# Kernel optimization log

Measured on AMD Instinct MI355X. Metric: run time of the kernel, lower is better.

Reference implementation:

```python
import jax, jax.numpy as jnp
import numpy as np

N, S, D = 8, 1024, 512      # batch, seq_len, in_dim
H, KD, VD, OD = 8, 64, 64, 512  # heads, key_dim, value_dim, out_dim
GRAPH_WEIGHT = 0.5
NEG_INF = float('-inf')


def setup_inputs() -> dict:
    key = jax.random.key(0)
    ks = jax.random.split(key, 9)
    return {
        "x":    jax.random.normal(ks[0], (N, S, D), jnp.float32),
        "Wk":   jax.random.normal(ks[1], (H, D, KD), jnp.float32) * 0.02,
        "bk":   jax.random.normal(ks[2], (H, KD), jnp.float32) * 0.02,
        "Wv":   jax.random.normal(ks[3], (H, D, VD), jnp.float32) * 0.02,
        "bv":   jax.random.normal(ks[4], (H, VD), jnp.float32) * 0.02,
        "Wout": jax.random.normal(ks[5], (H * VD, OD), jnp.float32) * 0.02,
        "bout": jax.random.normal(ks[6], (OD,), jnp.float32) * 0.02,
        "graph": jax.random.normal(ks[7], (S, S), jnp.float32),
        "knn": 64,
    }


def reference(x, Wk, bk, Wv, bv, Wout, bout, graph, knn):
    # Per-head key/value projections (heads vectorized on leading axis h).
    k = jnp.einsum('nsd,hdk->hnsk', x, Wk) + bk[:, None, None, :]   # (H,N,S,KD)
    v = jnp.einsum('nsd,hdv->hnsv', x, Wv) + bv[:, None, None, :]   # (H,N,S,VD)
    q = k  # self-attention: query = key

    # att_unnorm = (q . k) / sqrt(key_dim)  -> (H,N,S,S)
    att = jnp.einsum('hnqk,hntk->hnqt', q, k) / np.sqrt(KD).astype(np.float32)

    # Causal mask (equivalent to the Python loop att[:, i, i+1:] = -inf).
    causal = jnp.tril(jnp.ones((S, S), dtype=bool))
    att = jnp.where(causal, att, NEG_INF)

    # knn top-k pooling: keep top-knn entries along the last axis, rest -> -inf.
    topv = jax.lax.top_k(att, knn)[0]                  # (H,N,S,knn)
    kth = topv[..., -1:]                               # kth largest per row
    att = jnp.where(att >= kth, att, NEG_INF)

    p = jax.nn.softmax(att, axis=-1)

    # Graph-weighted attention blend (graph is row-softmaxed at init time).
    att_graph = jax.nn.softmax(graph, axis=-1)         # (S,S)
    p = GRAPH_WEIGHT * att_graph + (1.0 - GRAPH_WEIGHT) * p

    # y_h = att @ value, then concat heads and output projection.
    y = jnp.einsum('hnqt,hntv->hnqv', p, v)            # (H,N,S,VD)
    y = y.transpose(1, 2, 0, 3).reshape(N, S, H * VD)  # head-major concat
    return y @ Wout + bout
```

## Files before the change

kernel.cpp:

```cpp
#include <hip/hip_runtime.h>
#include <math.h>

#define NB 8
#define SL 1024
#define DI 512
#define HH 8
#define KDN 64
#define VDN 64
#define ODN 512
#define ATT_SCALE 0.125f

#define KLO_OFF 2097152u
#define V_OFF   4194304u
#define G_OFF   8388608u
#define Y_OFF   9437184u

#define ORD_NEG_INF 0x007FFFFFu

typedef __attribute__((ext_vector_type(8))) short bf16x8;
typedef __attribute__((ext_vector_type(4))) float f32x4;

__device__ __forceinline__ unsigned fordu(float f) {
  unsigned b = __float_as_uint(f);
  return b ^ ((b & 0x80000000u) ? 0xFFFFFFFFu : 0x80000000u);
}
__device__ __forceinline__ float ifordu(unsigned k) {
  unsigned b = k ^ ((k & 0x80000000u) ? 0x80000000u : 0xFFFFFFFFu);
  return __uint_as_float(b);
}
__device__ __forceinline__ unsigned short f2bf(float f) {
  unsigned u = __float_as_uint(f);
  unsigned r = (u + 0x7FFFu + ((u >> 16) & 1u)) >> 16;
  return (unsigned short)r;
}
__device__ __forceinline__ float bf2f(unsigned short h) {
  return __uint_as_float(((unsigned)h) << 16);
}

__global__ __launch_bounds__(256) void wprep_kernel(
    const float* __restrict__ Wk, const float* __restrict__ Wv, float* __restrict__ ws)
{
  __shared__ float tile[64][65];
  unsigned short* gbase = (unsigned short*)(ws + G_OFF);
  const int t = threadIdx.x;
  const int d0 = blockIdx.x * 64;
  const int hs = blockIdx.y;
  const int h = hs & 7, which = hs >> 3;
  const float* W = (which == 0) ? (Wk + (size_t)h * DI * KDN) : (Wv + (size_t)h * DI * VDN);
  unsigned short* whi = gbase + (size_t)which * 524288 + (size_t)h * KDN * DI;
  unsigned short* wlo = whi + 262144;
  const int r = t >> 2, c4 = (t & 3) * 16;
#pragma unroll
  for (int j = 0; j < 4; ++j)
    *(float4*)&tile[r][c4 + j * 4] = *(const float4*)&W[(size_t)(d0 + r) * KDN + c4 + j * 4];
  __syncthreads();
  union { unsigned short u[16]; uint4 v[2]; } hi, lo;
#pragma unroll
  for (int j = 0; j < 16; ++j) {
    const float f = tile[c4 + j][r];
    const unsigned short h16 = f2bf(f);
    hi.u[j] = h16;
    lo.u[j] = f2bf(f - bf2f(h16));
  }
  const size_t o = (size_t)r * DI + d0 + c4;
  *(uint4*)&whi[o] = hi.v[0];
  *(uint4*)&whi[o + 8] = hi.v[1];
  *(uint4*)&wlo[o] = lo.v[0];
  *(uint4*)&wlo[o + 8] = lo.v[1];
}

__global__ __launch_bounds__(256) void kvproj_kernel(
    const float* __restrict__ x, const float* __restrict__ bk,
    const float* __restrict__ bv, float* __restrict__ ws)
{
  const unsigned short* gbase = (const unsigned short*)(ws + G_OFF);
  const unsigned short* wkthi = gbase;
  const unsigned short* wktlo = gbase + 262144;
  const unsigned short* wvthi = gbase + 524288;
  const unsigned short* wvtlo = gbase + 786432;
  unsigned short* khi = (unsigned short*)ws;
  unsigned short* klo = (unsigned short*)(ws + KLO_OFF);
  float* vb = ws + V_OFF;

  const int tid = threadIdx.x;
  const int lane = tid & 63;
  const int wave = tid >> 6;
  const int col = lane & 15, grp = lane >> 4;
  const int m0 = blockIdx.x * 64;
  const int h = blockIdx.y;
  const int n = m0 >> 10, s0 = m0 & 1023;

  f32x4 ack[4], acv[4];
#pragma unroll
  for (int odt = 0; odt < 4; ++odt) { ack[odt] = (f32x4){0,0,0,0}; acv[odt] = (f32x4){0,0,0,0}; }

  const float* xrow = x + (size_t)(m0 + wave * 16 + col) * DI + grp * 8;
  for (int ks = 0; ks < 16; ++ks) {
    const float4 ya = *(const float4*)&xrow[ks * 32];
    const float4 yb = *(const float4*)&xrow[ks * 32 + 4];
    union { unsigned short u[8]; bf16x8 v; } ah, al;
    const float yf[8] = {ya.x, ya.y, ya.z, ya.w, yb.x, yb.y, yb.z, yb.w};
#pragma unroll
    for (int j = 0; j < 8; ++j) {
      const unsigned short h16 = f2bf(yf[j]);
      ah.u[j] = h16;
      al.u[j] = f2bf(yf[j] - bf2f(h16));
    }
#pragma unroll
    for (int odt = 0; odt < 4; ++odt) {
      const size_t bo = (size_t)(h * 64 + odt * 16 + col) * DI + ks * 32 + grp * 8;
      const bf16x8 kh = *(const bf16x8*)&wkthi[bo];
      const bf16x8 kl = *(const bf16x8*)&wktlo[bo];
      ack[odt] = __builtin_amdgcn_mfma_f32_16x16x32_bf16(ah.v, kh, ack[odt], 0, 0, 0);
      ack[odt] = __builtin_amdgcn_mfma_f32_16x16x32_bf16(ah.v, kl, ack[odt], 0, 0, 0);
      ack[odt] = __builtin_amdgcn_mfma_f32_16x16x32_bf16(al.v, kh, ack[odt], 0, 0, 0);
      const bf16x8 vh = *(const bf16x8*)&wvthi[bo];
      const bf16x8 vl = *(const bf16x8*)&wvtlo[bo];
      acv[odt] = __builtin_amdgcn_mfma_f32_16x16x32_bf16(ah.v, vh, acv[odt], 0, 0, 0);
      acv[odt] = __builtin_amdgcn_mfma_f32_16x16x32_bf16(ah.v, vl, acv[odt], 0, 0, 0);
      acv[odt] = __builtin_amdgcn_mfma_f32_16x16x32_bf16(al.v, vh, acv[odt], 0, 0, 0);
    }
  }

  const size_t hnbase = ((size_t)(h * NB + n) * SL);
#pragma unroll
  for (int odt = 0; odt < 4; ++odt) {
    const int kd = odt * 16 + col;
    const float bkv = bk[h * KDN + kd];
    const float bvv = bv[h * VDN + kd];
#pragma unroll
    for (int r = 0; r < 4; ++r) {
      const int s = s0 + wave * 16 + grp * 4 + r;
      const float kf = ack[odt][r] + bkv;
      const unsigned short h16 = f2bf(kf);
      khi[(hnbase + s) * KDN + kd] = h16;
      klo[(hnbase + s) * KDN + kd] = f2bf(kf - bf2f(h16));
      vb[(hnbase + s) * VDN + kd] = acv[odt][r] + bvv;
    }
  }
}

__global__ __launch_bounds__(256) void gsoftmax_kernel(const float* __restrict__ gin, float* __restrict__ ws)
{
  unsigned short* ghi = (unsigned short*)(ws + G_OFF);
  const int row = blockIdx.x;
  const int tid = threadIdx.x;
  const int lane = tid & 63, wave = tid >> 6;
  __shared__ float red[4];
  __shared__ float red2[4];
  float v[4];
  float m = -INFINITY;
#pragma unroll
  for (int i = 0; i < 4; ++i) {
    v[i] = gin[(size_t)row * SL + tid + i * 256];
    m = fmaxf(m, v[i]);
  }
#pragma unroll
  for (int off = 32; off; off >>= 1) m = fmaxf(m, __shfl_xor(m, off));
  if (lane == 0) red[wave] = m;
  __syncthreads();
  m = fmaxf(fmaxf(red[0], red[1]), fmaxf(red[2], red[3]));
  float e[4];
  float s = 0.f;
#pragma unroll
  for (int i = 0; i < 4; ++i) { e[i] = __expf(v[i] - m); s += e[i]; }
#pragma unroll
  for (int off = 32; off; off >>= 1) s += __shfl_xor(s, off);
  if (lane == 0) red2[wave] = s;
  __syncthreads();
  s = red2[0] + red2[1] + red2[2] + red2[3];
  const float inv = 1.0f / s;
#pragma unroll
  for (int i = 0; i < 4; ++i) ghi[(size_t)row * SL + tid + i * 256] = f2bf(e[i] * inv);
}

__global__ __launch_bounds__(512, 8) void attn_kernel(float* __restrict__ ws, const int* __restrict__ knn_p)
{
  __shared__ float S[16][260];
  const int tid = threadIdx.x;
  const int lane = tid & 63;
  const int wave = tid >> 6;
  const int q0 = blockIdx.x * 16;
  const int hn = blockIdx.y;
  const int h = hn >> 3, n = hn & 7;
  const int K = knn_p[0];
  const unsigned short* khi = (const unsigned short*)ws + (size_t)hn * SL * KDN;
  const unsigned short* klo = (const unsigned short*)(ws + KLO_OFF) + (size_t)hn * SL * KDN;
  const float* vb = ws + V_OFF + (size_t)hn * (SL * VDN);
  float* y = ws + Y_OFF;

  const int col = lane & 15, grp = lane >> 4;
  const bf16x8 a0h = *(const bf16x8*)&khi[(size_t)(q0 + col) * KDN + grp * 8];
  const bf16x8 a1h = *(const bf16x8*)&khi[(size_t)(q0 + col) * KDN + 32 + grp * 8];
  const bf16x8 a0l = *(const bf16x8*)&klo[(size_t)(q0 + col) * KDN + grp * 8];
  const bf16x8 a1l = *(const bf16x8*)&klo[(size_t)(q0 + col) * KDN + 32 + grp * 8];

  const int T = q0 / 16 + 1;
  const int rbase = wave * 2;

  float ev[2][8][2];
#pragma unroll
  for (int rr = 0; rr < 2; ++rr)
#pragma unroll
    for (int c = 0; c < 8; ++c) {
      ev[rr][c][0] = __uint_as_float(ORD_NEG_INF);
      ev[rr][c][1] = __uint_as_float(ORD_NEG_INF);
    }

#pragma unroll
  for (int ph = 0; ph < 4; ++ph) {
    const int tlo = ph * 16;
    const int thi = (T < tlo + 16) ? T : (tlo + 16);
    if (thi > tlo) {
      __syncthreads();
      for (int ti = tlo + wave; ti < thi; ti += 8) {
        const int t0 = ti * 16;
        const size_t bo = (size_t)(t0 + col) * KDN + grp * 8;
        const bf16x8 b0h = *(const bf16x8*)&khi[bo];
        const bf16x8 b1h = *(const bf16x8*)&khi[bo + 32];
        const bf16x8 b0l = *(const bf16x8*)&klo[bo];
        const bf16x8 b1l = *(const bf16x8*)&klo[bo + 32];
        f32x4 d = {0.f, 0.f, 0.f, 0.f};
        d = __builtin_amdgcn_mfma_f32_16x16x32_bf16(a0h, b0h, d, 0, 0, 0);
        d = __builtin_amdgcn_mfma_f32_16x16x32_bf16(a1h, b1h, d, 0, 0, 0);
        d = __builtin_amdgcn_mfma_f32_16x16x32_bf16(a0h, b0l, d, 0, 0, 0);
        d = __builtin_amdgcn_mfma_f32_16x16x32_bf16(a1h, b1l, d, 0, 0, 0);
        d = __builtin_amdgcn_mfma_f32_16x16x32_bf16(a0l, b0h, d, 0, 0, 0);
        d = __builtin_amdgcn_mfma_f32_16x16x32_bf16(a1l, b1h, d, 0, 0, 0);
        d = __builtin_amdgcn_mfma_f32_16x16x32_bf16(a0l, b0l, d, 0, 0, 0);
        d = __builtin_amdgcn_mfma_f32_16x16x32_bf16(a1l, b1l, d, 0, 0, 0);
        const int tl = t0 - ph * 256 + col;
#pragma unroll
        for (int r = 0; r < 4; ++r) S[grp * 4 + r][tl] = d[r];
      }
      __syncthreads();
#pragma unroll
      for (int rr = 0; rr < 2; ++rr) {
        const int q = q0 + rbase + rr;
        const int cmr = q >> 7;
#pragma unroll
        for (int cc = 0; cc < 2; ++cc) {
          const int c = ph * 2 + cc;
          if (c <= cmr) {
            const float2 sv = *(const float2*)&S[rbase + rr][cc * 128 + lane * 2];
            const int t0 = c * 128 + lane * 2;
            const unsigned k0 = (t0     <= q) ? fordu(sv.x * ATT_SCALE) : ORD_NEG_INF;
            const unsigned k1 = (t0 + 1 <= q) ? fordu(sv.y * ATT_SCALE) : ORD_NEG_INF;
            ev[rr][c][0] = __uint_as_float(k0);
            ev[rr][c][1] = __uint_as_float(k1);
          }
        }
      }
    }
  }
  __syncthreads();

  float* elist = (float*)((char*)&S[0][0] + wave * 768);
  unsigned short* tlist = (unsigned short*)(elist + 128);

#pragma unroll
  for (int rr = 0; rr < 2; ++rr) {
    const int q = q0 + rbase + rr;

    unsigned u[16];
#pragma unroll
    for (int c = 0; c < 8; ++c) {
      u[c * 2]     = __float_as_uint(ev[rr][c][0]);
      u[c * 2 + 1] = __float_as_uint(ev[rr][c][1]);
    }

    unsigned lmax = u[0];
#pragma unroll
    for (int i = 1; i < 16; ++i) lmax = lmax > u[i] ? lmax : u[i];
    unsigned mk = lmax, t0k = lmax;
#pragma unroll
    for (int off = 32; off; off >>= 1) {
      const unsigned om = (unsigned)__shfl_xor((int)mk, off);
      const unsigned ot = (unsigned)__shfl_xor((int)t0k, off);
      mk = mk > om ? mk : om;
      t0k = t0k < ot ? t0k : ot;
    }
    const float m = ifordu(mk);

    unsigned kth;
    if (q < K) {
      kth = ORD_NEG_INF;
    } else {
      unsigned lo = (K <= 64) ? t0k : 0u;
      unsigned hi = mk;
      while (lo < hi) {
        const unsigned mid = lo + ((hi - lo + 1) >> 1);
        int cnt = 0;
#pragma unroll
        for (int i = 0; i < 16; ++i)
          cnt += (int)__popcll(__ballot(u[i] >= mid));
        if (cnt >= K) lo = mid; else hi = mid - 1;
      }
      kth = lo;
    }

    float Z = 0.f;
#pragma unroll
    for (int c = 0; c < 8; ++c) {
#pragma unroll
      for (int j = 0; j < 2; ++j) {
        const unsigned k = u[c * 2 + j];
        float e = 0.f;
        if (k >= kth) e = __expf(ifordu(k) - m);
        ev[rr][c][j] = e;
        Z += e;
      }
    }
#pragma unroll
    for (int off = 32; off; off >>= 1) Z += __shfl_xor(Z, off);

    const unsigned long long lt = (1ull << lane) - 1ull;
    int cnt = 0;
#pragma unroll
    for (int c = 0; c < 8; ++c) {
#pragma unroll
      for (int j = 0; j < 2; ++j) {
        const float e = ev[rr][c][j];
        const unsigned long long msk = __ballot(e > 0.f);
        if (e > 0.f) {
          const int pos = cnt + (int)__popcll(msk & lt);
          if (pos < 128) {
            elist[pos] = e;
            tlist[pos] = (unsigned short)(c * 128 + lane * 2 + j);
          }
        }
        cnt += (int)__popcll(msk);
      }
    }
    cnt = (cnt < 128) ? cnt : 128;

    float yacc = 0.f;
    int i2 = 0;
    for (; i2 + 4 <= cnt; i2 += 4) {
      const float4 e4 = *(const float4*)&elist[i2];
      const ushort4 t4 = *(const ushort4*)&tlist[i2];
      yacc = __fmaf_rn(e4.x, vb[(size_t)t4.x * VDN + lane], yacc);
      yacc = __fmaf_rn(e4.y, vb[(size_t)t4.y * VDN + lane], yacc);
      yacc = __fmaf_rn(e4.z, vb[(size_t)t4.z * VDN + lane], yacc);
      yacc = __fmaf_rn(e4.w, vb[(size_t)t4.w * VDN + lane], yacc);
    }
    for (; i2 < cnt; ++i2) {
      yacc = __fmaf_rn(elist[i2], vb[(size_t)tlist[i2] * VDN + lane], yacc);
    }
    y[((size_t)(n * SL + q)) * ODN + h * VDN + lane] = yacc * (0.5f / Z);
  }
}

__global__ __launch_bounds__(256) void vtprep_kernel(float* __restrict__ ws)
{
  __shared__ float tile[64][65];
  const int t = threadIdx.x;
  const int t0 = blockIdx.x * 64;
  const int hn = blockIdx.y;
  const float* vb = ws + V_OFF + (size_t)hn * (SL * VDN);
  unsigned short* vthi = (unsigned short*)ws + (size_t)hn * VDN * SL;
  const int r = t >> 2, c4 = (t & 3) * 16;
#pragma unroll
  for (int j = 0; j < 4; ++j)
    *(float4*)&tile[r][c4 + j * 4] = *(const float4*)&vb[(size_t)(t0 + r) * VDN + c4 + j * 4];
  __syncthreads();
  union { unsigned short u[16]; uint4 v[2]; } hi;
#pragma unroll
  for (int j = 0; j < 16; ++j) hi.u[j] = f2bf(tile[c4 + j][r]);
  const size_t o = (size_t)r * SL + t0 + c4;
  *(uint4*)&vthi[o] = hi.v[0];
  *(uint4*)&vthi[o + 8] = hi.v[1];
}

__global__ __launch_bounds__(256) void gv_kernel(float* __restrict__ ws)
{
  const unsigned short* ghi = (const unsigned short*)(ws + G_OFF);
  const int tid = threadIdx.x;
  const int lane = tid & 63;
  const int wave = tid >> 6;
  const int col = lane & 15, grp = lane >> 4;
  const int q0 = blockIdx.x * 64;
  const int hn = blockIdx.y;
  const int h = hn >> 3, n = hn & 7;
  const unsigned short* vthi = (const unsigned short*)ws + (size_t)hn * VDN * SL;
  float* y = ws + Y_OFF;

  f32x4 acc[4];
#pragma unroll
  for (int odt = 0; odt < 4; ++odt) acc[odt] = (f32x4){0.f, 0.f, 0.f, 0.f};

  const size_t arow = (size_t)(q0 + wave * 16 + col) * SL;
  for (int ks = 0; ks < 32; ++ks) {
    const bf16x8 ah = *(const bf16x8*)&ghi[arow + ks * 32 + grp * 8];
#pragma unroll
    for (int odt = 0; odt < 4; ++odt) {
      const bf16x8 bh = *(const bf16x8*)&vthi[(size_t)(odt * 16 + col) * SL + ks * 32 + grp * 8];
      acc[odt] = __builtin_amdgcn_mfma_f32_16x16x32_bf16(ah, bh, acc[odt], 0, 0, 0);
    }
  }

#pragma unroll
  for (int odt = 0; odt < 4; ++odt) {
    const int vd = odt * 16 + col;
#pragma unroll
    for (int r = 0; r < 4; ++r) {
      const size_t off = ((size_t)(n * SL + q0 + wave * 16 + grp * 4 + r)) * ODN + h * VDN + vd;
      y[off] += 0.5f * acc[odt][r];
    }
  }
}

__global__ __launch_bounds__(256) void wtprep_kernel(const float* __restrict__ Wout, float* __restrict__ ws)
{
  __shared__ float tile[64][65];
  unsigned short* wth = (unsigned short*)(ws + KLO_OFF);
  unsigned short* wtl = wth + ODN * ODN;
  const int t = threadIdx.x;
  const int od0 = blockIdx.x * 64;
  const int k0 = blockIdx.y * 64;
  const int r = t >> 2, c4 = (t & 3) * 16;
#pragma unroll
  for (int j = 0; j < 4; ++j) {
    *(float4*)&tile[r][c4 + j * 4] = *(const float4*)&Wout[(size_t)(k0 + r) * ODN + od0 + c4 + j * 4];
  }
  __syncthreads();
  union { unsigned short u[16]; uint4 v[2]; } hi, lo;
#pragma unroll
  for (int j = 0; j < 16; ++j) {
    const float f = tile[c4 + j][r];
    const unsigned short h16 = f2bf(f);
    hi.u[j] = h16;
    lo.u[j] = f2bf(f - bf2f(h16));
  }
  const size_t o = (size_t)(od0 + r) * ODN + k0 + c4;
  *(uint4*)&wth[o] = hi.v[0];
  *(uint4*)&wth[o + 8] = hi.v[1];
  *(uint4*)&wtl[o] = lo.v[0];
  *(uint4*)&wtl[o + 8] = lo.v[1];
}

__global__ __launch_bounds__(256) void out_kernel(
    const float* __restrict__ bout, const float* __restrict__ ws, float* __restrict__ out)
{
  const unsigned short* wth = (const unsigned short*)(ws + KLO_OFF);
  const unsigned short* wtl = wth + ODN * ODN;
  const float* y = ws + Y_OFF;
  const int tid = threadIdx.x;
  const int lane = tid & 63;
  const int wave = tid >> 6;
  const int col = lane & 15, grp = lane >> 4;
  const int od0 = blockIdx.x * 64;
  const int m0 = blockIdx.y * 64 + wave * 16;

  f32x4 acc[4];
#pragma unroll
  for (int odt = 0; odt < 4; ++odt) acc[odt] = (f32x4){0.f, 0.f, 0.f, 0.f};

  const float* yrow = y + (size_t)(m0 + col) * ODN + grp * 8;
  for (int ks = 0; ks < 16; ++ks) {
    const float4 ya = *(const float4*)&yrow[ks * 32];
    const float4 yb = *(const float4*)&yrow[ks * 32 + 4];
    union { unsigned short u[8]; bf16x8 v; } ah, al;
    const float yf[8] = {ya.x, ya.y, ya.z, ya.w, yb.x, yb.y, yb.z, yb.w};
#pragma unroll
    for (int j = 0; j < 8; ++j) {
      const unsigned short h16 = f2bf(yf[j]);
      ah.u[j] = h16;
      al.u[j] = f2bf(yf[j] - bf2f(h16));
    }
#pragma unroll
    for (int odt = 0; odt < 4; ++odt) {
      const size_t bo = (size_t)(od0 + odt * 16 + col) * ODN + ks * 32 + grp * 8;
      const bf16x8 bh = *(const bf16x8*)&wth[bo];
      const bf16x8 bl = *(const bf16x8*)&wtl[bo];
      acc[odt] = __builtin_amdgcn_mfma_f32_16x16x32_bf16(ah.v, bh, acc[odt], 0, 0, 0);
      acc[odt] = __builtin_amdgcn_mfma_f32_16x16x32_bf16(ah.v, bl, acc[odt], 0, 0, 0);
      acc[odt] = __builtin_amdgcn_mfma_f32_16x16x32_bf16(al.v, bh, acc[odt], 0, 0, 0);
    }
  }

#pragma unroll
  for (int odt = 0; odt < 4; ++odt) {
    const int od = od0 + odt * 16 + col;
    const float bo = bout[od];
#pragma unroll
    for (int r = 0; r < 4; ++r) {
      out[(size_t)(m0 + grp * 4 + r) * ODN + od] = acc[odt][r] + bo;
    }
  }
}

extern "C" void kernel_launch(void* const* d_in, const int* in_sizes, int n_in,
                              void* d_out, int out_size, void* d_ws, size_t ws_size,
                              hipStream_t stream)
{
  const float* x     = (const float*)d_in[0];
  const float* Wk    = (const float*)d_in[1];
  const float* bk    = (const float*)d_in[2];
  const float* Wv    = (const float*)d_in[3];
  const float* bv    = (const float*)d_in[4];
  const float* Wout  = (const float*)d_in[5];
  const float* bout  = (const float*)d_in[6];
  const float* graph = (const float*)d_in[7];
  const int*   knn   = (const int*)d_in[8];
  float* out = (float*)d_out;
  float* ws  = (float*)d_ws;

  wprep_kernel<<<dim3(8, 16), 256, 0, stream>>>(Wk, Wv, ws);
  kvproj_kernel<<<dim3(128, 8), 256, 0, stream>>>(x, bk, bv, ws);
  gsoftmax_kernel<<<dim3(1024), 256, 0, stream>>>(graph, ws);
  attn_kernel<<<dim3(64, 64), 512, 0, stream>>>(ws, knn);
  vtprep_kernel<<<dim3(16, 64), 256, 0, stream>>>(ws);
  wtprep_kernel<<<dim3(8, 8), 256, 0, stream>>>(Wout, ws);
  gv_kernel<<<dim3(16, 64), 256, 0, stream>>>(ws);
  out_kernel<<<dim3(8, 128), 256, 0, stream>>>(bout, ws, out);
}
```

Measured before the change: 520.2 us.

## Fuse V transpose into kvproj, store V in bf16, defer exp to kept entries

The kvproj kernel now stages the hi/lo bf16 split of x in shared memory and writes V directly as bf16 in both row-major and transposed layouts, so the separate vtprep kernel and its fp32 V round trip are gone. The attention kernel gathers bf16 V values, which halves gather bytes but lowers V precision from fp32 to bf16 in the sparse path. Exponentials are computed only for the compacted kept entries instead of all 16 per lane, which cuts per-row transcendental work and register use. The added shared-memory staging and extra syncs in kvproj could offset some of the savings.

Measured after the change: 511.6 us. Within noise of the previous version (-1.7%).

```diff
diff --git a/kernel.cpp b/kernel.cpp
--- a/kernel.cpp
+++ b/kernel.cpp
@@ -69,10 +69,11 @@
   *(uint4*)&wlo[o + 8] = lo.v[1];
 }
 
-__global__ __launch_bounds__(256) void kvproj_kernel(
+__global__ __launch_bounds__(256, 4) void kvproj_kernel(
     const float* __restrict__ x, const float* __restrict__ bk,
     const float* __restrict__ bv, float* __restrict__ ws)
 {
+  __shared__ unsigned short xsplit[2][64][72];
   const unsigned short* gbase = (const unsigned short*)(ws + G_OFF);
   const unsigned short* wkthi = gbase;
   const unsigned short* wktlo = gbase + 262144;
@@ -80,7 +81,6 @@
   const unsigned short* wvtlo = gbase + 786432;
   unsigned short* khi = (unsigned short*)ws;
   unsigned short* klo = (unsigned short*)(ws + KLO_OFF);
-  float* vb = ws + V_OFF;
 
   const int tid = threadIdx.x;
   const int lane = tid & 63;
@@ -94,35 +94,55 @@
 #pragma unroll
   for (int odt = 0; odt < 4; ++odt) { ack[odt] = (f32x4){0,0,0,0}; acv[odt] = (f32x4){0,0,0,0}; }
 
-  const float* xrow = x + (size_t)(m0 + wave * 16 + col) * DI + grp * 8;
-  for (int ks = 0; ks < 16; ++ks) {
-    const float4 ya = *(const float4*)&xrow[ks * 32];
-    const float4 yb = *(const float4*)&xrow[ks * 32 + 4];
-    union { unsigned short u[8]; bf16x8 v; } ah, al;
-    const float yf[8] = {ya.x, ya.y, ya.z, ya.w, yb.x, yb.y, yb.z, yb.w};
-#pragma unroll
-    for (int j = 0; j < 8; ++j) {
-      const unsigned short h16 = f2bf(yf[j]);
-      ah.u[j] = h16;
-      al.u[j] = f2bf(yf[j] - bf2f(h16));
-    }
-#pragma unroll
-    for (int odt = 0; odt < 4; ++odt) {
-      const size_t bo = (size_t)(h * 64 + odt * 16 + col) * DI + ks * 32 + grp * 8;
-      const bf16x8 kh = *(const bf16x8*)&wkthi[bo];
-      const bf16x8 kl = *(const bf16x8*)&wktlo[bo];
-      ack[odt] = __builtin_amdgcn_mfma_f32_16x16x32_bf16(ah.v, kh, ack[odt], 0, 0, 0);
-      ack[odt] = __builtin_amdgcn_mfma_f32_16x16x32_bf16(ah.v, kl, ack[odt], 0, 0, 0);
-      ack[odt] = __builtin_amdgcn_mfma_f32_16x16x32_bf16(al.v, kh, ack[odt], 0, 0, 0);
-      const bf16x8 vh = *(const bf16x8*)&wvthi[bo];
-      const bf16x8 vl = *(const bf16x8*)&wvtlo[bo];
-      acv[odt] = __builtin_amdgcn_mfma_f32_16x16x32_bf16(ah.v, vh, acv[odt], 0, 0, 0);
-      acv[odt] = __builtin_amdgcn_mfma_f32_16x16x32_bf16(ah.v, vl, acv[odt], 0, 0, 0);
-      acv[odt] = __builtin_amdgcn_mfma_f32_16x16x32_bf16(al.v, vh, acv[odt], 0, 0, 0);
-    }
-  }
-
-  const size_t hnbase = ((size_t)(h * NB + n) * SL);
+  const int sr = tid >> 2;
+  const int sc = (tid & 3) * 16;
+
+  for (int dt = 0; dt < 8; ++dt) {
+    __syncthreads();
+    {
+      const float* xrow = &x[(size_t)(m0 + sr) * DI + dt * 64 + sc];
+      union { unsigned short u[16]; uint4 v[2]; } hi, lo;
+#pragma unroll
+      for (int j4 = 0; j4 < 4; ++j4) {
+        const float4 xv = *(const float4*)&xrow[j4 * 4];
+        const float xf[4] = {xv.x, xv.y, xv.z, xv.w};
+#pragma unroll
+        for (int j = 0; j < 4; ++j) {
+          const unsigned short h16 = f2bf(xf[j]);
+          hi.u[j4 * 4 + j] = h16;
+          lo.u[j4 * 4 + j] = f2bf(xf[j] - bf2f(h16));
+        }
+      }
+      *(uint4*)&xsplit[0][sr][sc]     = hi.v[0];
+      *(uint4*)&xsplit[0][sr][sc + 8] = hi.v[1];
+      *(uint4*)&xsplit[1][sr][sc]     = lo.v[0];
+      *(uint4*)&xsplit[1][sr][sc + 8] = lo.v[1];
+    }
+    __syncthreads();
+#pragma unroll
+    for (int half = 0; half < 2; ++half) {
+      const bf16x8 ah = *(const bf16x8*)&xsplit[0][wave * 16 + col][half * 32 + grp * 8];
+      const bf16x8 al = *(const bf16x8*)&xsplit[1][wave * 16 + col][half * 32 + grp * 8];
+#pragma unroll
+      for (int odt = 0; odt < 4; ++odt) {
+        const size_t bo = (size_t)(h * 64 + odt * 16 + col) * DI + dt * 64 + half * 32 + grp * 8;
+        const bf16x8 kh = *(const bf16x8*)&wkthi[bo];
+        const bf16x8 kl = *(const bf16x8*)&wktlo[bo];
+        ack[odt] = __builtin_amdgcn_mfma_f32_16x16x32_bf16(ah, kh, ack[odt], 0, 0, 0);
+        ack[odt] = __builtin_amdgcn_mfma_f32_16x16x32_bf16(ah, kl, ack[odt], 0, 0, 0);
+        ack[odt] = __builtin_amdgcn_mfma_f32_16x16x32_bf16(al, kh, ack[odt], 0, 0, 0);
+        const bf16x8 vh = *(const bf16x8*)&wvthi[bo];
+        const bf16x8 vl = *(const bf16x8*)&wvtlo[bo];
+        acv[odt] = __builtin_amdgcn_mfma_f32_16x16x32_bf16(ah, vh, acv[odt], 0, 0, 0);
+        acv[odt] = __builtin_amdgcn_mfma_f32_16x16x32_bf16(ah, vl, acv[odt], 0, 0, 0);
+        acv[odt] = __builtin_amdgcn_mfma_f32_16x16x32_bf16(al, vh, acv[odt], 0, 0, 0);
+      }
+    }
+  }
+
+  const size_t hnbase = (size_t)(h * NB + n) * SL;
+  __syncthreads();
+  float* vtile = (float*)xsplit;
 #pragma unroll
   for (int odt = 0; odt < 4; ++odt) {
     const int kd = odt * 16 + col;
@@ -130,13 +150,32 @@
     const float bvv = bv[h * VDN + kd];
 #pragma unroll
     for (int r = 0; r < 4; ++r) {
-      const int s = s0 + wave * 16 + grp * 4 + r;
+      const int sl = wave * 16 + grp * 4 + r;
+      const int s = s0 + sl;
       const float kf = ack[odt][r] + bkv;
       const unsigned short h16 = f2bf(kf);
       khi[(hnbase + s) * KDN + kd] = h16;
       klo[(hnbase + s) * KDN + kd] = f2bf(kf - bf2f(h16));
-      vb[(hnbase + s) * VDN + kd] = acv[odt][r] + bvv;
-    }
+      vtile[sl * 72 + kd] = acv[odt][r] + bvv;
+    }
+  }
+  __syncthreads();
+  {
+    unsigned short* vbf = (unsigned short*)(ws + V_OFF);
+    unsigned short* vtb = vbf + 4194304u;
+    union { unsigned short u[16]; uint4 v[2]; } pv, pt;
+#pragma unroll
+    for (int j = 0; j < 16; ++j) {
+      pv.u[j] = f2bf(vtile[sr * 72 + sc + j]);
+      pt.u[j] = f2bf(vtile[(sc + j) * 72 + sr]);
+    }
+    unsigned short* vrow = &vbf[(hnbase + s0 + sr) * VDN];
+    *(uint4*)&vrow[sc] = pv.v[0];
+    *(uint4*)&vrow[sc + 8] = pv.v[1];
+    unsigned short* vt = vtb + hnbase * VDN;
+    const size_t o = (size_t)sr * SL + s0 + sc;
+    *(uint4*)&vt[o] = pt.v[0];
+    *(uint4*)&vt[o + 8] = pt.v[1];
   }
 }
 
@@ -186,7 +225,7 @@
   const int K = knn_p[0];
   const unsigned short* khi = (const unsigned short*)ws + (size_t)hn * SL * KDN;
   const unsigned short* klo = (const unsigned short*)(ws + KLO_OFF) + (size_t)hn * SL * KDN;
-  const float* vb = ws + V_OFF + (size_t)hn * (SL * VDN);
+  const unsigned short* vb = (const unsigned short*)(ws + V_OFF) + (size_t)hn * (SL * VDN);
   float* y = ws + Y_OFF;
 
   const int col = lane & 15, grp = lane >> 4;
@@ -262,16 +301,14 @@
   for (int rr = 0; rr < 2; ++rr) {
     const int q = q0 + rbase + rr;
 
-    unsigned u[16];
+    unsigned lmax = __float_as_uint(ev[rr][0][0]);
 #pragma unroll
     for (int c = 0; c < 8; ++c) {
-      u[c * 2]     = __float_as_uint(ev[rr][c][0]);
-      u[c * 2 + 1] = __float_as_uint(ev[rr][c][1]);
-    }
-
-    unsigned lmax = u[0];
-#pragma unroll
-    for (int i = 1; i < 16; ++i) lmax = lmax > u[i] ? lmax : u[i];
+      const unsigned a = __float_as_uint(ev[rr][c][0]);
+      const unsigned b = __float_as_uint(ev[rr][c][1]);
+      lmax = lmax > a ? lmax : a;
+      lmax = lmax > b ? lmax : b;
+    }
     unsigned mk = lmax, t0k = lmax;
 #pragma unroll
     for (int off = 32; off; off >>= 1) {
@@ -292,40 +329,28 @@
         const unsigned mid = lo + ((hi - lo + 1) >> 1);
         int cnt = 0;
 #pragma unroll
-        for (int i = 0; i < 16; ++i)
-          cnt += (int)__popcll(__ballot(u[i] >= mid));
+        for (int c = 0; c < 8; ++c) {
+          cnt += (int)__popcll(__ballot(__float_as_uint(ev[rr][c][0]) >= mid));
+          cnt += (int)__popcll(__ballot(__float_as_uint(ev[rr][c][1]) >= mid));
+        }
         if (cnt >= K) lo = mid; else hi = mid - 1;
       }
       kth = lo;
     }
 
-    float Z = 0.f;
-#pragma unroll
-    for (int c = 0; c < 8; ++c) {
-#pragma unroll
-      for (int j = 0; j < 2; ++j) {
-        const unsigned k = u[c * 2 + j];
-        float e = 0.f;
-        if (k >= kth) e = __expf(ifordu(k) - m);
-        ev[rr][c][j] = e;
-        Z += e;
-      }
-    }
-#pragma unroll
-    for (int off = 32; off; off >>= 1) Z += __shfl_xor(Z, off);
-
     const unsigned long long lt = (1ull << lane) - 1ull;
     int cnt = 0;
 #pragma unroll
     for (int c = 0; c < 8; ++c) {
 #pragma unroll
       for (int j = 0; j < 2; ++j) {
-        const float e = ev[rr][c][j];
-        const unsigned long long msk = __ballot(e > 0.f);
-        if (e > 0.f) {
+        const unsigned k = __float_as_uint(ev[rr][c][j]);
+        const bool keep = (k >= kth) && (k != ORD_NEG_INF);
+        const unsigned long long msk = __ballot(keep);
+        if (keep) {
           const int pos = cnt + (int)__popcll(msk & lt);
           if (pos < 128) {
-            elist[pos] = e;
+            elist[pos] = ev[rr][c][j];
             tlist[pos] = (unsigned short)(c * 128 + lane * 2 + j);
           }
         }
@@ -334,42 +359,40 @@
     }
     cnt = (cnt < 128) ? cnt : 128;
 
+    float zp = 0.f;
+    if (lane < cnt) {
+      const float e = __expf(ifordu(__float_as_uint(elist[lane])) - m);
+      elist[lane] = e;
+      zp += e;
+    }
+    if (lane + 64 < cnt) {
+      const float e = __expf(ifordu(__float_as_uint(elist[lane + 64])) - m);
+      elist[lane + 64] = e;
+      zp += e;
+    }
+    float Z = zp;
+#pragma unroll
+    for (int off = 32; off; off >>= 1) Z += __shfl_xor(Z, off);
+
     float yacc = 0.f;
     int i2 = 0;
     for (; i2 + 4 <= cnt; i2 += 4) {
       const float4 e4 = *(const float4*)&elist[i2];
       const ushort4 t4 = *(const ushort4*)&tlist[i2];
-      yacc = __fmaf_rn(e4.x, vb[(size_t)t4.x * VDN + lane], yacc);
-      yacc = __fmaf_rn(e4.y, vb[(size_t)t4.y * VDN + lane], yacc);
-      yacc = __fmaf_rn(e4.z, vb[(size_t)t4.z * VDN + lane], yacc);
-      yacc = __fmaf_rn(e4.w, vb[(size_t)t4.w * VDN + lane], yacc);
+      const float v0 = bf2f(vb[(size_t)t4.x * VDN + lane]);
+      const float v1 = bf2f(vb[(size_t)t4.y * VDN + lane]);
+      const float v2 = bf2f(vb[(size_t)t4.z * VDN + lane]);
+      const float v3 = bf2f(vb[(size_t)t4.w * VDN + lane]);
+      yacc = __fmaf_rn(e4.x, v0, yacc);
+      yacc = __fmaf_rn(e4.y, v1, yacc);
+      yacc = __fmaf_rn(e4.z, v2, yacc);
+      yacc = __fmaf_rn(e4.w, v3, yacc);
     }
     for (; i2 < cnt; ++i2) {
-      yacc = __fmaf_rn(elist[i2], vb[(size_t)tlist[i2] * VDN + lane], yacc);
+      yacc = __fmaf_rn(elist[i2], bf2f(vb[(size_t)tlist[i2] * VDN + lane]), yacc);
     }
     y[((size_t)(n * SL + q)) * ODN + h * VDN + lane] = yacc * (0.5f / Z);
   }
-}
-
-__global__ __launch_bounds__(256) void vtprep_kernel(float* __restrict__ ws)
-{
-  __shared__ float tile[64][65];
-  const int t = threadIdx.x;
-  const int t0 = blockIdx.x * 64;
-  const int hn = blockIdx.y;
-  const float* vb = ws + V_OFF + (size_t)hn * (SL * VDN);
-  unsigned short* vthi = (unsigned short*)ws + (size_t)hn * VDN * SL;
-  const int r = t >> 2, c4 = (t & 3) * 16;
-#pragma unroll
-  for (int j = 0; j < 4; ++j)
-    *(float4*)&tile[r][c4 + j * 4] = *(const float4*)&vb[(size_t)(t0 + r) * VDN + c4 + j * 4];
-  __syncthreads();
-  union { unsigned short u[16]; uint4 v[2]; } hi;
-#pragma unroll
-  for (int j = 0; j < 16; ++j) hi.u[j] = f2bf(tile[c4 + j][r]);
-  const size_t o = (size_t)r * SL + t0 + c4;
-  *(uint4*)&vthi[o] = hi.v[0];
-  *(uint4*)&vthi[o + 8] = hi.v[1];
 }
 
 __global__ __launch_bounds__(256) void gv_kernel(float* __restrict__ ws)
@@ -382,7 +405,7 @@
   const int q0 = blockIdx.x * 64;
   const int hn = blockIdx.y;
   const int h = hn >> 3, n = hn & 7;
-  const unsigned short* vthi = (const unsigned short*)ws + (size_t)hn * VDN * SL;
+  const unsigned short* vthi = (const unsigned short*)(ws + V_OFF) + 4194304u + (size_t)hn * VDN * SL;
   float* y = ws + Y_OFF;
 
   f32x4 acc[4];
@@ -510,7 +533,6 @@
   kvproj_kernel<<<dim3(128, 8), 256, 0, stream>>>(x, bk, bv, ws);
   gsoftmax_kernel<<<dim3(1024), 256, 0, stream>>>(graph, ws);
   attn_kernel<<<dim3(64, 64), 512, 0, stream>>>(ws, knn);
-  vtprep_kernel<<<dim3(16, 64), 256, 0, stream>>>(ws);
   wtprep_kernel<<<dim3(8, 8), 256, 0, stream>>>(Wout, ws);
   gv_kernel<<<dim3(16, 64), 256, 0, stream>>>(ws);
   out_kernel<<<dim3(8, 128), 256, 0, stream>>>(bout, ws, out);
```
